# Optimization experiments

Measured on AMD Instinct MI355X. Metric: run time of the kernel, lower is better.

## Reference

```python
import jax, jax.numpy as jnp
import numpy as np

N = 100000
IN_DIM = 128
HID = 256
OUT_DIM = 128
E = 600000


def setup_inputs() -> dict:
    key = jax.random.key(0)
    ks = jax.random.split(key, 10)
    x = jax.random.normal(ks[0], (N, IN_DIM), dtype=jnp.float32)
    edge_index = jax.random.randint(ks[1], (2, E), 0, N, dtype=jnp.int32)

    def lin(k, fan_in, fan_out):
        kw, kb = jax.random.split(k)
        bound = 1.0 / np.sqrt(fan_in)
        W = jax.random.uniform(kw, (fan_in, fan_out), minval=-bound, maxval=bound, dtype=jnp.float32)
        b = jax.random.uniform(kb, (fan_out,), minval=-bound, maxval=bound, dtype=jnp.float32)
        return W, b

    W1a, b1a = lin(ks[2], IN_DIM, HID)
    W1b, b1b = lin(ks[3], HID, HID)
    W2a, b2a = lin(ks[4], HID, HID)
    W2b, b2b = lin(ks[5], HID, OUT_DIM)
    return {"x": x, "edge_index": edge_index,
            "W1a": W1a, "b1a": b1a, "W1b": W1b, "b1b": b1b,
            "W2a": W2a, "b2a": b2a, "W2b": W2b, "b2b": b2b}


def _gin_conv(x, src, dst, Wa, ba, Wb, bb):
    # GINConv with eps=0: h = (1+eps)*x + sum_{j in N(i)} x_j, then 2-layer MLP
    agg = jax.ops.segment_sum(x[src], dst, num_segments=N)  # [N, F]
    h = x + agg
    h = jax.nn.relu(h @ Wa + ba)
    return h @ Wb + bb


def reference(x, edge_index, W1a, b1a, W1b, b1b, W2a, b2a, W2b, b2b):
    src, dst = edge_index[0], edge_index[1]
    h = jax.nn.relu(_gin_conv(x, src, dst, W1a, b1a, W1b, b1b))
    h = jax.nn.relu(_gin_conv(h, src, dst, W2a, b2a, W2b, b2b))
    return h
```

## Files before the change

kernel.cpp:

```cpp
#include <hip/hip_runtime.h>
#include <stdint.h>

#define N_NODES 100000
#define E_EDGES 600000
#define IN_F    128
#define HID_F   256
#define OUT_F   128
#define NB_SCAN 98

typedef unsigned short ushort_t;
typedef short  short8  __attribute__((ext_vector_type(8)));
typedef float  floatx4 __attribute__((ext_vector_type(4)));

__device__ __forceinline__ float bf2f(unsigned u16) {
    return __uint_as_float(u16 << 16);
}
__device__ __forceinline__ ushort_t f2bf(float f) {
    unsigned u = __float_as_uint(f);
    return (ushort_t)((u + 0x7fffu + ((u >> 16) & 1u)) >> 16);
}

__global__ void k_prep(const float* __restrict__ x, ushort_t* __restrict__ xbf,
                       const float* __restrict__ W1a, const float* __restrict__ W1b,
                       const float* __restrict__ W2a, const float* __restrict__ W2b,
                       ushort_t* __restrict__ WT1a, ushort_t* __restrict__ WT1b,
                       ushort_t* __restrict__ WT2a, ushort_t* __restrict__ WT2b,
                       int* __restrict__ cursor) {
    int t = blockIdx.x * 256 + threadIdx.x;
    if (t < N_NODES * IN_F / 2) {
        float2 v = ((const float2*)x)[t];
        ((unsigned*)xbf)[t] = (unsigned)f2bf(v.x) | ((unsigned)f2bf(v.y) << 16);
    }
    if (t < N_NODES) cursor[t] = 0;
    if (t < 32768) {
        int k = t >> 8, n = t & 255;
        WT1a[n * 128 + k] = f2bf(W1a[t]);
    } else if (t < 98304) {
        int i = t - 32768, k = i >> 8, n = i & 255;
        WT1b[n * 256 + k] = f2bf(W1b[i]);
    } else if (t < 163840) {
        int i = t - 98304, k = i >> 8, n = i & 255;
        WT2a[n * 256 + k] = f2bf(W2a[i]);
    } else if (t < 196608) {
        int i = t - 163840, k = i >> 7, n = i & 127;
        WT2b[n * 256 + k] = f2bf(W2b[i]);
    }
}

__global__ void k_hist(const int* __restrict__ dst, int* __restrict__ deg) {
    int e = blockIdx.x * 256 + threadIdx.x;
    if (e < E_EDGES) atomicAdd(&deg[dst[e]], 1);
}

__global__ void k_scan1(const int* __restrict__ deg, int* __restrict__ row_ptr,
                        int* __restrict__ psum) {
    __shared__ int s[1024];
    int t = threadIdx.x, i = blockIdx.x * 1024 + t;
    int v = (i < N_NODES) ? deg[i] : 0;
    s[t] = v;
    __syncthreads();
    for (int off = 1; off < 1024; off <<= 1) {
        int u = (t >= off) ? s[t - off] : 0;
        __syncthreads();
        if (t >= off) s[t] += u;
        __syncthreads();
    }
    if (i < N_NODES) row_ptr[i] = s[t] - v;
    if (t == 1023) psum[blockIdx.x] = s[t];
}

__global__ void k_scan2(int* __restrict__ psum) {
    __shared__ int s[128];
    int t = threadIdx.x;
    int v = (t < NB_SCAN) ? psum[t] : 0;
    s[t] = v;
    __syncthreads();
    for (int off = 1; off < 128; off <<= 1) {
        int u = (t >= off) ? s[t - off] : 0;
        __syncthreads();
        if (t >= off) s[t] += u;
        __syncthreads();
    }
    if (t < NB_SCAN) psum[t] = s[t] - v;
}

__global__ void k_scan3(int* __restrict__ row_ptr, const int* __restrict__ psum,
                        int* __restrict__ cursor) {
    int i = blockIdx.x * 1024 + threadIdx.x;
    if (i < N_NODES) {
        int r = row_ptr[i] + psum[i >> 10];
        row_ptr[i] = r;
        cursor[i]  = r;
    }
    if (i == 0) row_ptr[N_NODES] = E_EDGES;
}

__global__ void k_fill(const int* __restrict__ src, const int* __restrict__ dst,
                       int* __restrict__ cursor, int* __restrict__ colidx) {
    int e = blockIdx.x * 256 + threadIdx.x;
    if (e < E_EDGES) {
        int pos = atomicAdd(&cursor[dst[e]], 1);
        colidx[pos] = src[e];
    }
}

__global__ void k_agg128(const ushort_t* __restrict__ Xbf, const int* __restrict__ row_ptr,
                         const int* __restrict__ colidx, ushort_t* __restrict__ Out) {
    int node = blockIdx.x * 4 + (threadIdx.x >> 6);
    int lane = threadIdx.x & 63;
    const unsigned* xr = (const unsigned*)Xbf;
    unsigned u = xr[node * 64 + lane];
    float a0 = bf2f(u & 0xffffu), a1 = bf2f(u >> 16);
    int r0 = row_ptr[node], r1 = row_ptr[node + 1];
    int r = r0;
    for (; r + 4 <= r1; r += 4) {
        int j0 = colidx[r], j1 = colidx[r + 1], j2 = colidx[r + 2], j3 = colidx[r + 3];
        unsigned w0 = xr[j0 * 64 + lane];
        unsigned w1 = xr[j1 * 64 + lane];
        unsigned w2 = xr[j2 * 64 + lane];
        unsigned w3 = xr[j3 * 64 + lane];
        a0 += (bf2f(w0 & 0xffffu) + bf2f(w1 & 0xffffu)) +
              (bf2f(w2 & 0xffffu) + bf2f(w3 & 0xffffu));
        a1 += (bf2f(w0 >> 16) + bf2f(w1 >> 16)) +
              (bf2f(w2 >> 16) + bf2f(w3 >> 16));
    }
    for (; r < r1; ++r) {
        int j = colidx[r];
        unsigned w = xr[j * 64 + lane];
        a0 += bf2f(w & 0xffffu);
        a1 += bf2f(w >> 16);
    }
    ((unsigned*)Out)[node * 64 + lane] =
        (unsigned)f2bf(a0) | ((unsigned)f2bf(a1) << 16);
}

__global__ void k_agg256(const ushort_t* __restrict__ X, const int* __restrict__ row_ptr,
                         const int* __restrict__ colidx, ushort_t* __restrict__ Out) {
    int node = blockIdx.x * 4 + (threadIdx.x >> 6);
    int lane = threadIdx.x & 63;
    const uint2* xr = (const uint2*)X;
    uint2 u = xr[node * 64 + lane];
    float a0 = bf2f(u.x & 0xffffu), a1 = bf2f(u.x >> 16);
    float a2 = bf2f(u.y & 0xffffu), a3 = bf2f(u.y >> 16);
    int r0 = row_ptr[node], r1 = row_ptr[node + 1];
    int r = r0;
    for (; r + 4 <= r1; r += 4) {
        int j0 = colidx[r], j1 = colidx[r + 1], j2 = colidx[r + 2], j3 = colidx[r + 3];
        uint2 w0 = xr[j0 * 64 + lane];
        uint2 w1 = xr[j1 * 64 + lane];
        uint2 w2 = xr[j2 * 64 + lane];
        uint2 w3 = xr[j3 * 64 + lane];
        a0 += (bf2f(w0.x & 0xffffu) + bf2f(w1.x & 0xffffu)) +
              (bf2f(w2.x & 0xffffu) + bf2f(w3.x & 0xffffu));
        a1 += (bf2f(w0.x >> 16) + bf2f(w1.x >> 16)) +
              (bf2f(w2.x >> 16) + bf2f(w3.x >> 16));
        a2 += (bf2f(w0.y & 0xffffu) + bf2f(w1.y & 0xffffu)) +
              (bf2f(w2.y & 0xffffu) + bf2f(w3.y & 0xffffu));
        a3 += (bf2f(w0.y >> 16) + bf2f(w1.y >> 16)) +
              (bf2f(w2.y >> 16) + bf2f(w3.y >> 16));
    }
    for (; r < r1; ++r) {
        int j = colidx[r];
        uint2 w = xr[j * 64 + lane];
        a0 += bf2f(w.x & 0xffffu); a1 += bf2f(w.x >> 16);
        a2 += bf2f(w.y & 0xffffu); a3 += bf2f(w.y >> 16);
    }
    uint2 o;
    o.x = (unsigned)f2bf(a0) | ((unsigned)f2bf(a1) << 16);
    o.y = (unsigned)f2bf(a2) | ((unsigned)f2bf(a3) << 16);
    ((uint2*)Out)[node * 64 + lane] = o;
}

template <int FIN, int FOUT, bool OUT_F32>
__global__ __launch_bounds__(512, 4) void gemm_relu(
    const ushort_t* __restrict__ Act, const ushort_t* __restrict__ WT,
    const float* __restrict__ bias, void* __restrict__ Out, int nRows)
{
    constexpr int CPR = FIN / 8;
    constexpr int KC  = FIN / 32;
    constexpr int KH  = (KC > 4) ? 4 : KC;
    __shared__ ushort_t wt[128 * FIN];

    const int tid  = threadIdx.x;
    const int slab = blockIdx.y * 128;

    {
        const ushort_t* wsrc = WT + (size_t)slab * FIN;
#pragma unroll
        for (int rr = 0; rr < (128 * CPR) / 512; ++rr) {
            int ci  = rr * 512 + tid;
            int n   = ci / CPR;
            int csw = ci % CPR;
            int cor = csw ^ (n & 15);
            uint4 v = *(const uint4*)(wsrc + (size_t)n * FIN + cor * 8);
            *(uint4*)&wt[ci * 8] = v;
        }
    }

    const int wave = tid >> 6, lane = tid & 63;
    const int quad = lane >> 4, l15 = lane & 15;
    const int rowBase = blockIdx.x * 256 + wave * 32;

    int r0 = rowBase + l15;
    int r1 = r0 + 16;
    r0 = (r0 < nRows) ? r0 : (nRows - 1);
    r1 = (r1 < nRows) ? r1 : (nRows - 1);
    const ushort_t* a0p = Act + (size_t)r0 * FIN + quad * 8;
    const ushort_t* a1p = Act + (size_t)r1 * FIN + quad * 8;

    short8 af[2][KH];
#pragma unroll
    for (int kc = 0; kc < KH; ++kc) {
        af[0][kc] = *(const short8*)(a0p + kc * 32);
        af[1][kc] = *(const short8*)(a1p + kc * 32);
    }

    floatx4 acc[2][8];
#pragma unroll
    for (int mt = 0; mt < 2; ++mt)
#pragma unroll
        for (int nt = 0; nt < 8; ++nt)
#pragma unroll
            for (int r = 0; r < 4; ++r) acc[mt][nt][r] = 0.f;

    __syncthreads();

#pragma unroll
    for (int half = 0; half < KC / KH; ++half) {
        if (half > 0) {
#pragma unroll
            for (int kc = 0; kc < KH; ++kc) {
                af[0][kc] = *(const short8*)(a0p + (KH + kc) * 32);
                af[1][kc] = *(const short8*)(a1p + (KH + kc) * 32);
            }
        }
#pragma unroll
        for (int kc = 0; kc < KH; ++kc) {
            int chunk = (half * KH + kc) * 4 + quad;
#pragma unroll
            for (int nt = 0; nt < 8; ++nt) {
                int n = nt * 16 + l15;
                int csw = chunk ^ (n & 15);
                short8 bfr = *(const short8*)&wt[n * FIN + csw * 8];
                acc[0][nt] = __builtin_amdgcn_mfma_f32_16x16x32_bf16(af[0][kc], bfr, acc[0][nt], 0, 0, 0);
                acc[1][nt] = __builtin_amdgcn_mfma_f32_16x16x32_bf16(af[1][kc], bfr, acc[1][nt], 0, 0, 0);
            }
        }
    }

#pragma unroll
    for (int mt = 0; mt < 2; ++mt) {
#pragma unroll
        for (int nt = 0; nt < 8; ++nt) {
            int col = slab + nt * 16 + l15;
            float bv = bias[col];
#pragma unroll
            for (int r = 0; r < 4; ++r) {
                int row = rowBase + mt * 16 + quad * 4 + r;
                if (row < nRows) {
                    float v = fmaxf(acc[mt][nt][r] + bv, 0.f);
                    if (OUT_F32)
                        ((float*)Out)[(size_t)row * FOUT + col] = v;
                    else
                        ((ushort_t*)Out)[(size_t)row * FOUT + col] = f2bf(v);
                }
            }
        }
    }
}

extern "C" void kernel_launch(void* const* d_in, const int* in_sizes, int n_in,
                              void* d_out, int out_size, void* d_ws, size_t ws_size,
                              hipStream_t stream) {
    const float* x   = (const float*)d_in[0];
    const int*   ei  = (const int*)d_in[1];
    const int*   src = ei;
    const int*   dst = ei + E_EDGES;
    const float* W1a = (const float*)d_in[2];
    const float* b1a = (const float*)d_in[3];
    const float* W1b = (const float*)d_in[4];
    const float* b1b = (const float*)d_in[5];
    const float* W2a = (const float*)d_in[6];
    const float* b2a = (const float*)d_in[7];
    const float* W2b = (const float*)d_in[8];
    const float* b2b = (const float*)d_in[9];

    ushort_t* P       = (ushort_t*)d_ws;
    ushort_t* Q       = P + (size_t)N_NODES * HID_F;
    ushort_t* xbf     = Q;
    int*      row_ptr = (int*)(Q + (size_t)N_NODES * HID_F);
    int*      cursor  = row_ptr + (N_NODES + 4);
    int*      colidx  = cursor + N_NODES;
    int*      psum    = colidx + E_EDGES;
    ushort_t* WT1a    = (ushort_t*)(psum + 128);
    ushort_t* WT1b    = WT1a + 256 * 128;
    ushort_t* WT2a    = WT1b + 256 * 256;
    ushort_t* WT2b    = WT2a + 256 * 256;

    k_prep<<<(N_NODES * IN_F / 2 + 255) / 256, 256, 0, stream>>>(
        x, xbf, W1a, W1b, W2a, W2b, WT1a, WT1b, WT2a, WT2b, cursor);

    k_hist <<<(E_EDGES + 255) / 256, 256, 0, stream>>>(dst, cursor);
    k_scan1<<<NB_SCAN, 1024, 0, stream>>>(cursor, row_ptr, psum);
    k_scan2<<<1, 128, 0, stream>>>(psum);
    k_scan3<<<NB_SCAN, 1024, 0, stream>>>(row_ptr, psum, cursor);
    k_fill <<<(E_EDGES + 255) / 256, 256, 0, stream>>>(src, dst, cursor, colidx);

    const int ROWB = (N_NODES + 255) / 256;

    k_agg128<<<N_NODES / 4, 256, 0, stream>>>(xbf, row_ptr, colidx, P);
    gemm_relu<128, 256, false><<<dim3(ROWB, 2), 512, 0, stream>>>(P, WT1a, b1a, Q, N_NODES);
    gemm_relu<256, 256, false><<<dim3(ROWB, 2), 512, 0, stream>>>(Q, WT1b, b1b, P, N_NODES);

    k_agg256<<<N_NODES / 4, 256, 0, stream>>>(P, row_ptr, colidx, Q);
    gemm_relu<256, 256, false><<<dim3(ROWB, 2), 512, 0, stream>>>(Q, WT2a, b2a, P, N_NODES);
    gemm_relu<256, 128, true><<<dim3(ROWB, 1), 512, 0, stream>>>(P, WT2b, b2b, d_out, N_NODES);
}
```

Baseline: 403.3 us.

## Load GEMM weights directly into LDS and double-buffer activation fragments

The weight slab now moves from global memory into LDS with the global_load_lds builtin, skipping the trip through VGPRs. Activation fragments are loaded in pairs of K-chunks with a two-stage register double buffer, so the next pair is fetched while MFMAs run on the current one. The aim is to hide global load latency behind matrix math and to reduce register pressure. The direct-to-LDS path depends on the builtin writing to the expected per-lane LDS addresses, so the swizzled layout could be wrong if that does not hold.

```diff
diff --git a/kernel.cpp b/kernel.cpp
--- a/kernel.cpp
+++ b/kernel.cpp
@@ -178,7 +178,7 @@
 {
     constexpr int CPR = FIN / 8;
     constexpr int KC  = FIN / 32;
-    constexpr int KH  = (KC > 4) ? 4 : KC;
+    constexpr int KP  = KC / 2;
     __shared__ ushort_t wt[128 * FIN];
 
     const int tid  = threadIdx.x;
@@ -192,8 +192,11 @@
             int n   = ci / CPR;
             int csw = ci % CPR;
             int cor = csw ^ (n & 15);
-            uint4 v = *(const uint4*)(wsrc + (size_t)n * FIN + cor * 8);
-            *(uint4*)&wt[ci * 8] = v;
+            const ushort_t* g = wsrc + (size_t)n * FIN + cor * 8;
+            __builtin_amdgcn_global_load_lds(
+                (const __attribute__((address_space(1))) unsigned*)g,
+                (__attribute__((address_space(3))) unsigned*)&wt[ci * 8],
+                16, 0, 0);
         }
     }
 
@@ -208,11 +211,11 @@
     const ushort_t* a0p = Act + (size_t)r0 * FIN + quad * 8;
     const ushort_t* a1p = Act + (size_t)r1 * FIN + quad * 8;
 
-    short8 af[2][KH];
-#pragma unroll
-    for (int kc = 0; kc < KH; ++kc) {
-        af[0][kc] = *(const short8*)(a0p + kc * 32);
-        af[1][kc] = *(const short8*)(a1p + kc * 32);
+    short8 af[2][2][2];
+#pragma unroll
+    for (int kc = 0; kc < 2; ++kc) {
+        af[0][0][kc] = *(const short8*)(a0p + kc * 32);
+        af[0][1][kc] = *(const short8*)(a1p + kc * 32);
     }
 
     floatx4 acc[2][8];
@@ -226,24 +229,25 @@
     __syncthreads();
 
 #pragma unroll
-    for (int half = 0; half < KC / KH; ++half) {
-        if (half > 0) {
-#pragma unroll
-            for (int kc = 0; kc < KH; ++kc) {
-                af[0][kc] = *(const short8*)(a0p + (KH + kc) * 32);
-                af[1][kc] = *(const short8*)(a1p + (KH + kc) * 32);
+    for (int p = 0; p < KP; ++p) {
+        const int cb = p & 1, nb = cb ^ 1;
+        if (p + 1 < KP) {
+#pragma unroll
+            for (int kc = 0; kc < 2; ++kc) {
+                af[nb][0][kc] = *(const short8*)(a0p + ((p + 1) * 2 + kc) * 32);
+                af[nb][1][kc] = *(const short8*)(a1p + ((p + 1) * 2 + kc) * 32);
             }
         }
 #pragma unroll
-        for (int kc = 0; kc < KH; ++kc) {
-            int chunk = (half * KH + kc) * 4 + quad;
+        for (int kc = 0; kc < 2; ++kc) {
+            int chunk = (p * 2 + kc) * 4 + quad;
 #pragma unroll
             for (int nt = 0; nt < 8; ++nt) {
                 int n = nt * 16 + l15;
                 int csw = chunk ^ (n & 15);
                 short8 bfr = *(const short8*)&wt[n * FIN + csw * 8];
-                acc[0][nt] = __builtin_amdgcn_mfma_f32_16x16x32_bf16(af[0][kc], bfr, acc[0][nt], 0, 0, 0);
-                acc[1][nt] = __builtin_amdgcn_mfma_f32_16x16x32_bf16(af[1][kc], bfr, acc[1][nt], 0, 0, 0);
+                acc[0][nt] = __builtin_amdgcn_mfma_f32_16x16x32_bf16(af[cb][0][kc], bfr, acc[0][nt], 0, 0, 0);
+                acc[1][nt] = __builtin_amdgcn_mfma_f32_16x16x32_bf16(af[cb][1][kc], bfr, acc[1][nt], 0, 0, 0);
             }
         }
     }
```

After: 402.1 us. Within noise of the previous version (-0.3%).
